# Kernel tuning notes

Hardware: AMD Instinct MI355X
Metric: run time of the kernel (lower is better)

Reference implementation:

```python
import jax, jax.numpy as jnp
import numpy as np

N = 100000   # nodes
E = 600000   # edges
IN = 128     # in_channels
H = 128      # hidden_channels
C = 47       # num_classes
L = 3        # num_layers
EPS = 1e-5   # batchnorm eps


def setup_inputs() -> dict:
    key = jax.random.key(0)
    ks = jax.random.split(key, 18)
    s = 0.05
    f = jnp.float32
    return {
        "x": jax.random.normal(ks[0], (N, IN), f),
        "in_W": jax.random.normal(ks[1], (IN, H), f) * s,
        "in_b": jnp.zeros((H,), f),
        "ibn_g": jnp.ones((H,), f),
        "ibn_b": jnp.zeros((H,), f),
        "ibn_m": jax.random.normal(ks[2], (H,), f) * 0.1,
        "ibn_v": jax.random.uniform(ks[3], (H,), f, 0.5, 1.5),
        "Wl": jax.random.normal(ks[4], (L, H, H), f) * s,   # SAGEConv lin_l (on aggregated neighbors)
        "bl": jnp.zeros((L, H), f),
        "Wr": jax.random.normal(ks[5], (L, H, H), f) * s,   # SAGEConv lin_r (root weight, no bias)
        "bn_g": jnp.ones((L, H), f),
        "bn_b": jnp.zeros((L, H), f),
        "bn_m": jax.random.normal(ks[6], (L, H), f) * 0.1,
        "bn_v": jax.random.uniform(ks[7], (L, H), f, 0.5, 1.5),
        "out_W": jax.random.normal(ks[8], (H, C), f) * s,
        "out_b": jnp.zeros((C,), f),
        "edge_index": jax.random.randint(ks[9], (2, E), 0, N),
    }


def _bn(h, g, b, m, v):
    # inference-mode BatchNorm1d with running stats
    return (h - m) * (g * jax.lax.rsqrt(v + EPS)) + b


def _sage(x, src, dst, Wl, bl, Wr):
    # mean aggregation of source features at destination nodes (PyG SAGEConv)
    msg = x[src]                                                   # [E, H] gather
    agg = jax.ops.segment_sum(msg, dst, num_segments=N)            # [N, H] scatter-add
    cnt = jax.ops.segment_sum(jnp.ones((src.shape[0],), x.dtype), dst, num_segments=N)
    agg = agg / jnp.maximum(cnt, 1.0)[:, None]                     # segment mean
    return agg @ Wl + bl + x @ Wr


def reference(x, in_W, in_b, ibn_g, ibn_b, ibn_m, ibn_v, Wl, bl, Wr,
              bn_g, bn_b, bn_m, bn_v, out_W, out_b, edge_index):
    src, dst = edge_index[0], edge_index[1]
    h = jax.nn.relu(_bn(x @ in_W + in_b, ibn_g, ibn_b, ibn_m, ibn_v))
    for l in range(L):  # small fixed layer count
        t = _sage(h, src, dst, Wl[l], bl[l], Wr[l])
        t = jax.nn.relu(_bn(t, bn_g[l], bn_b[l], bn_m[l], bn_v[l]))
        h = h + t  # residual
    return h @ out_W + out_b
```

## Files before the change

kernel.cpp:

```cpp
#include <hip/hip_runtime.h>
#include <math.h>

#define NN 100000
#define NE 600000
#define HD 128
#define NC 47
#define NL 3
#define BEPS 1e-5f

typedef unsigned short u16;
typedef unsigned int u32;
typedef __attribute__((ext_vector_type(8))) short bf16x8;
typedef __attribute__((ext_vector_type(4))) float f32x4;

__device__ inline u16 f2b(float f) {
  u32 u = __float_as_uint(f);
  u += 0x7fff + ((u >> 16) & 1);
  return (u16)(u >> 16);
}
__device__ inline float b2f(u16 us) { return __uint_as_float(((u32)us) << 16); }

__device__ inline void load_lds16(const void* g, void* l) {
  __builtin_amdgcn_global_load_lds(
      (const __attribute__((address_space(1))) void*)g,
      (__attribute__((address_space(3))) void*)l, 16, 0, 0);
}


__global__ void k_zero2(int* __restrict__ a, int* __restrict__ b) {
  int i = blockIdx.x * blockDim.x + threadIdx.x;
  if (i < NN) { a[i] = 0; b[i] = 0; }
}

__global__ void k_hist(const int* __restrict__ dst, int* __restrict__ cnt) {
  int e = blockIdx.x * blockDim.x + threadIdx.x;
  if (e < NE) atomicAdd(&cnt[dst[e]], 1);
}

__global__ void k_scan1(const int* __restrict__ cnt, int* __restrict__ rs, int* __restrict__ part) {
  __shared__ int s[256];
  int tid = threadIdx.x;
  int base = blockIdx.x * 1024;
  int i0 = base + tid * 4;
  int c[4];
#pragma unroll
  for (int j = 0; j < 4; j++) c[j] = (i0 + j < NN) ? cnt[i0 + j] : 0;
  int tsum = c[0] + c[1] + c[2] + c[3];
  s[tid] = tsum;
  __syncthreads();
  for (int off = 1; off < 256; off <<= 1) {
    int v = (tid >= off) ? s[tid - off] : 0;
    __syncthreads();
    s[tid] += v;
    __syncthreads();
  }
  int run = s[tid] - tsum;
#pragma unroll
  for (int j = 0; j < 4; j++) {
    run += c[j];
    if (i0 + j < NN) rs[i0 + j + 1] = run;
  }
  if (tid == 255) part[blockIdx.x] = s[255];
}

__global__ void k_scan2(const int* __restrict__ part, int* __restrict__ offs, int nb, int* __restrict__ rs) {
  __shared__ int s[128];
  int tid = threadIdx.x;
  int v = (tid < nb) ? part[tid] : 0;
  s[tid] = v;
  __syncthreads();
  for (int off = 1; off < 128; off <<= 1) {
    int u = (tid >= off) ? s[tid - off] : 0;
    __syncthreads();
    s[tid] += u;
    __syncthreads();
  }
  if (tid < nb) offs[tid] = s[tid] - v;
  if (tid == 0) rs[0] = 0;
}

__global__ void k_scan3(int* __restrict__ rs, const int* __restrict__ offs) {
  int off = offs[blockIdx.x];
  int base = blockIdx.x * 1024;
  int tid = threadIdx.x;
#pragma unroll
  for (int j = 0; j < 4; j++) {
    int i = base + tid * 4 + j;
    if (i < NN) rs[i + 1] += off;
  }
}

__global__ void k_scatter(const int* __restrict__ src, const int* __restrict__ dstA,
                          const int* __restrict__ rs, int* __restrict__ cur, int* __restrict__ ssrc) {
  int e = blockIdx.x * blockDim.x + threadIdx.x;
  if (e < NE) {
    int d = dstA[e];
    int p = atomicAdd(&cur[d], 1);
    ssrc[rs[d] + p] = src[e];
  }
}


__global__ void k_pack_all(const float* __restrict__ inW, const float* __restrict__ Wl,
                           const float* __restrict__ Wr, const float* __restrict__ oW,
                           u16* __restrict__ wpin, u16* __restrict__ wpl, u16* __restrict__ wpo) {
  int bid = blockIdx.x;
  int lane = threadIdx.x;
  int g = lane >> 4, r = lane & 15;
  union { u16 u[8]; uint4 v; } o;
  if (bid < 32) {
    int kt = bid >> 3, nt = bid & 7;
#pragma unroll
    for (int j = 0; j < 8; j++) {
      int k = kt * 32 + g * 8 + j, n = nt * 16 + r;
      o.u[j] = f2b(inW[k * HD + n]);
    }
    *(uint4*)(wpin + ((size_t)bid * 64 + lane) * 8) = o.v;
  } else if (bid < 224) {
    int b2 = bid - 32;
    int l = b2 >> 6, T = b2 & 63;
    int kt = T >> 3, nt = T & 7;
    const float* wl = Wl + (size_t)l * HD * HD;
    const float* wr = Wr + (size_t)l * HD * HD;
#pragma unroll
    for (int j = 0; j < 8; j++) {
      int k = kt * 32 + g * 8 + j, n = nt * 16 + r;
      o.u[j] = f2b(k < HD ? wl[k * HD + n] : wr[(k - HD) * HD + n]);
    }
    *(uint4*)(wpl + (((size_t)l * 64 + T) * 64 + lane) * 8) = o.v;
  } else {
    int T = bid - 224;
    int kt = T / 3, nt = T % 3;
#pragma unroll
    for (int j = 0; j < 8; j++) {
      int k = kt * 32 + g * 8 + j, n = nt * 16 + r;
      o.u[j] = (n < NC) ? f2b(oW[k * NC + n]) : (u16)0;
    }
    *(uint4*)(wpo + ((size_t)T * 64 + lane) * 8) = o.v;
  }
}


__global__ void k_agg(const u16* __restrict__ h, const int* __restrict__ rs,
                      const int* __restrict__ ssrc, u16* __restrict__ agg) {
  int gw = (blockIdx.x * blockDim.x + threadIdx.x) >> 6;
  int lane = threadIdx.x & 63;
  if (gw >= NN) return;
  int s = rs[gw], e = rs[gw + 1];
  const u32* h32 = (const u32*)h;
  float a0 = 0.f, a1 = 0.f, b0 = 0.f, b1 = 0.f;
  float c0 = 0.f, c1 = 0.f, d0 = 0.f, d1 = 0.f;
  int p = s;
  for (; p + 4 <= e; p += 4) {
    int n0 = ssrc[p], n1 = ssrc[p + 1], n2 = ssrc[p + 2], n3 = ssrc[p + 3];
    u32 u0 = h32[(size_t)n0 * 64 + lane];
    u32 u1 = h32[(size_t)n1 * 64 + lane];
    u32 u2 = h32[(size_t)n2 * 64 + lane];
    u32 u3 = h32[(size_t)n3 * 64 + lane];
    a0 += b2f((u16)(u0 & 0xffff)); a1 += b2f((u16)(u0 >> 16));
    b0 += b2f((u16)(u1 & 0xffff)); b1 += b2f((u16)(u1 >> 16));
    c0 += b2f((u16)(u2 & 0xffff)); c1 += b2f((u16)(u2 >> 16));
    d0 += b2f((u16)(u3 & 0xffff)); d1 += b2f((u16)(u3 >> 16));
  }
  if (p + 2 <= e) {
    int n0 = ssrc[p], n1 = ssrc[p + 1];
    u32 u0 = h32[(size_t)n0 * 64 + lane];
    u32 u1 = h32[(size_t)n1 * 64 + lane];
    a0 += b2f((u16)(u0 & 0xffff)); a1 += b2f((u16)(u0 >> 16));
    b0 += b2f((u16)(u1 & 0xffff)); b1 += b2f((u16)(u1 >> 16));
    p += 2;
  }
  if (p < e) {
    int n0 = ssrc[p];
    u32 u0 = h32[(size_t)n0 * 64 + lane];
    a0 += b2f((u16)(u0 & 0xffff)); a1 += b2f((u16)(u0 >> 16));
  }
  a0 += b0 + c0 + d0;
  a1 += b1 + c1 + d1;
  float inv = 1.0f / (float)max(e - s, 1);
  u32 o = (u32)f2b(a0 * inv) | ((u32)f2b(a1 * inv) << 16);
  ((u32*)agg)[(size_t)gw * 64 + lane] = o;
}


template <int KS, int MODE>
__global__ __launch_bounds__(256, 4) void k_mm(
    const float* __restrict__ Af, const u16* __restrict__ A0, const u16* __restrict__ A1,
    const u16* __restrict__ Wp, u16* __restrict__ hout,
    const float* __restrict__ bias, const float* __restrict__ g,
    const float* __restrict__ bb, const float* __restrict__ m,
    const float* __restrict__ v) {
  __shared__ __align__(1024) char As_raw[64 * KS * 64];
  __shared__ float sc_s[HD], sh_s[HD];
  int tid = threadIdx.x;
  int lane = tid & 63;
  int w = tid >> 6;
  long rbase = (long)blockIdx.x * 64;

  if (tid < HD) {
    float sc = g[tid] * rsqrtf(v[tid] + BEPS);
    sc_s[tid] = sc;
    sh_s[tid] = (bias[tid] - m[tid]) * sc + bb[tid];
  }

  if constexpr (MODE == 1) {
#pragma unroll
    for (int t = 0; t < 8; t++) {
      int op = w * 8 + t;
      int rowL = op * 2 + (lane >> 5);
      int p = lane & 31;
      int q = (p & 16) | ((p & 15) ^ (rowL & 15));
      long rg = rbase + rowL; if (rg > NN - 1) rg = NN - 1;
      const char* src = (q < 16)
          ? (const char*)A0 + rg * 256 + (size_t)q * 16
          : (const char*)A1 + rg * 256 + (size_t)(q - 16) * 16;
      load_lds16(src, As_raw + (size_t)op * 1024);
    }
  } else {
    int row = tid >> 2;
    int cq = (tid & 3) * 4;
    long rg = rbase + row; if (rg > NN - 1) rg = NN - 1;
    const float* srcp = Af + rg * HD + cq * 8;
#pragma unroll
    for (int ch = 0; ch < 4; ch++) {
      float4 f0 = *(const float4*)(srcp + ch * 8);
      float4 f1 = *(const float4*)(srcp + ch * 8 + 4);
      union { u16 u[8]; uint4 v4; } o;
      o.u[0] = f2b(f0.x); o.u[1] = f2b(f0.y); o.u[2] = f2b(f0.z); o.u[3] = f2b(f0.w);
      o.u[4] = f2b(f1.x); o.u[5] = f2b(f1.y); o.u[6] = f2b(f1.z); o.u[7] = f2b(f1.w);
      int q = cq + ch;
      int p = q ^ (row & 15);
      *(uint4*)(As_raw + (size_t)row * 256 + (size_t)p * 16) = o.v4;
    }
  }
  __syncthreads();

  int nb = w * 32;
  f32x4 acc[4][2];
#pragma unroll
  for (int mi = 0; mi < 4; mi++)
#pragma unroll
    for (int ni = 0; ni < 2; ni++) acc[mi][ni] = (f32x4)(0.0f);

#pragma unroll
  for (int kt = 0; kt < KS; kt++) {
    bf16x8 bfr[2];
#pragma unroll
    for (int ni = 0; ni < 2; ni++)
      bfr[ni] = *(const bf16x8*)(Wp + (((size_t)kt * 8 + (w * 2 + ni)) * 64 + lane) * 8);
#pragma unroll
    for (int mi = 0; mi < 4; mi++) {
      int row = mi * 16 + (lane & 15);
      int slot = kt * 4 + (lane >> 4);
      int p = (slot & ~15) | ((slot & 15) ^ (row & 15));
      bf16x8 afr = *(const bf16x8*)(As_raw + (size_t)row * (KS * 64) + (size_t)p * 16);
#pragma unroll
      for (int ni = 0; ni < 2; ni++)
        acc[mi][ni] = __builtin_amdgcn_mfma_f32_16x16x32_bf16(afr, bfr[ni], acc[mi][ni], 0, 0, 0);
    }
  }

#pragma unroll
  for (int mi = 0; mi < 4; mi++) {
#pragma unroll
    for (int ni = 0; ni < 2; ni++) {
      int c = nb + ni * 16 + (lane & 15);
      float sc = sc_s[c], sh = sh_s[c];
#pragma unroll
      for (int r = 0; r < 4; r++) {
        int rowL = mi * 16 + (lane >> 4) * 4 + r;
        long rg = rbase + rowL;
        if (rg >= NN) continue;
        float val = fmaxf(acc[mi][ni][r] * sc + sh, 0.f);
        if constexpr (MODE == 1) {
          int p = 16 | ((c >> 3) ^ (rowL & 15));
          u16 ho = *(const u16*)(As_raw + (size_t)rowL * 512 + (size_t)p * 16 + (c & 7) * 2);
          val += b2f(ho);
        }
        hout[rg * HD + c] = f2b(val);
      }
    }
  }
}


__global__ __launch_bounds__(256, 4) void k_outmm(const u16* __restrict__ h,
                                                  const u16* __restrict__ Wp,
                                                  const float* __restrict__ ob,
                                                  float* __restrict__ outp) {
  __shared__ __align__(1024) char As_raw[64 * 256];
  int tid = threadIdx.x;
  int lane = tid & 63;
  int w = tid >> 6;
  long rbase = (long)blockIdx.x * 64;
#pragma unroll
  for (int t = 0; t < 4; t++) {
    int op = w * 4 + t;
    int rowL = op * 4 + (lane >> 4);
    int p = lane & 15;
    int q = p ^ (rowL & 15);
    long rg = rbase + rowL; if (rg > NN - 1) rg = NN - 1;
    load_lds16((const char*)h + rg * 256 + (size_t)q * 16, As_raw + (size_t)op * 1024);
  }
  __syncthreads();

  f32x4 acc[3];
#pragma unroll
  for (int nt = 0; nt < 3; nt++) acc[nt] = (f32x4)(0.0f);
  int rowb = w * 16;
#pragma unroll
  for (int kt = 0; kt < 4; kt++) {
    int row = rowb + (lane & 15);
    int slot = kt * 4 + (lane >> 4);
    int p = slot ^ (row & 15);
    bf16x8 afr = *(const bf16x8*)(As_raw + (size_t)row * 256 + (size_t)p * 16);
#pragma unroll
    for (int nt = 0; nt < 3; nt++) {
      bf16x8 bfr = *(const bf16x8*)(Wp + (((size_t)kt * 3 + nt) * 64 + lane) * 8);
      acc[nt] = __builtin_amdgcn_mfma_f32_16x16x32_bf16(afr, bfr, acc[nt], 0, 0, 0);
    }
  }
#pragma unroll
  for (int nt = 0; nt < 3; nt++) {
#pragma unroll
    for (int r = 0; r < 4; r++) {
      long rg = rbase + rowb + (lane >> 4) * 4 + r;
      int c = nt * 16 + (lane & 15);
      if (rg < NN && c < NC) outp[rg * NC + c] = acc[nt][r] + ob[c];
    }
  }
}


extern "C" void kernel_launch(void* const* d_in, const int* in_sizes, int n_in,
                              void* d_out, int out_size, void* d_ws, size_t ws_size,
                              hipStream_t stream) {
  const float* x     = (const float*)d_in[0];
  const float* in_W  = (const float*)d_in[1];
  const float* in_b  = (const float*)d_in[2];
  const float* ibn_g = (const float*)d_in[3];
  const float* ibn_b = (const float*)d_in[4];
  const float* ibn_m = (const float*)d_in[5];
  const float* ibn_v = (const float*)d_in[6];
  const float* Wl    = (const float*)d_in[7];
  const float* bl    = (const float*)d_in[8];
  const float* Wr    = (const float*)d_in[9];
  const float* bn_g  = (const float*)d_in[10];
  const float* bn_b  = (const float*)d_in[11];
  const float* bn_m  = (const float*)d_in[12];
  const float* bn_v  = (const float*)d_in[13];
  const float* oW    = (const float*)d_in[14];
  const float* ob    = (const float*)d_in[15];
  const int* ei      = (const int*)d_in[16];
  const int* srcA = ei;
  const int* dstA = ei + NE;
  float* outp = (float*)d_out;

  char* W = (char*)d_ws;
  u16* h    = (u16*)W;
  u16* agg  = (u16*)(W + 25600000);
  u16* wpin = (u16*)(W + 76800000);
  u16* wpl  = (u16*)(W + 76800000 + 32768);
  u16* wpo  = (u16*)(W + 76800000 + 32768 + 196608);
  int* rs   = (int*)(W + 77041664);
  int* cnt  = rs + (NN + 1);
  int* cur  = cnt + NN;
  int* ssrc = cur + NN;
  int* part = ssrc + NE;
  int* offs = part + 128;

  k_zero2<<<(NN + 255) / 256, 256, 0, stream>>>(cnt, cur);
  k_hist<<<(NE + 255) / 256, 256, 0, stream>>>(dstA, cnt);
  int nb1 = (NN + 1023) / 1024;
  k_scan1<<<nb1, 256, 0, stream>>>(cnt, rs, part);
  k_scan2<<<1, 128, 0, stream>>>(part, offs, nb1, rs);
  k_scan3<<<nb1, 256, 0, stream>>>(rs, offs);
  k_scatter<<<(NE + 255) / 256, 256, 0, stream>>>(srcA, dstA, rs, cur, ssrc);

  k_pack_all<<<236, 64, 0, stream>>>(in_W, Wl, Wr, oW, wpin, wpl, wpo);

  int gblocks = (NN + 63) / 64;
  k_mm<4, 0><<<gblocks, 256, 0, stream>>>(x, nullptr, nullptr, wpin, h,
                                          in_b, ibn_g, ibn_b, ibn_m, ibn_v);
  for (int l = 0; l < NL; ++l) {
    k_agg<<<NN / 4, 256, 0, stream>>>(h, rs, ssrc, agg);
    k_mm<8, 1><<<gblocks, 256, 0, stream>>>(nullptr, agg, h, wpl + (size_t)l * 64 * 512, h,
                                            bl + (size_t)l * HD, bn_g + (size_t)l * HD,
                                            bn_b + (size_t)l * HD, bn_m + (size_t)l * HD,
                                            bn_v + (size_t)l * HD);
  }
  k_outmm<<<gblocks, 256, 0, stream>>>(h, wpo, ob, outp);
}
```

Before: 381.6 us.

## Partition CSR build atomics by destination range and aggregate four nodes per wave

The histogram and scatter kernels now use grid-stride loops in which each of eight block groups handles only destinations in its own range of 12500 nodes. The intent is to localize atomics and writes per group, at the cost of every group reading the whole destination array. The aggregation kernel now processes four destination nodes per wavefront and interleaves their neighbor gathers to expose more memory-level parallelism. This adds divergence when the four nodes have very different degrees and reduces the wave count.

New measurement: 427.0 us. +11.9%, slower.

```diff
diff --git a/kernel.cpp b/kernel.cpp
--- a/kernel.cpp
+++ b/kernel.cpp
@@ -32,9 +32,16 @@
   if (i < NN) { a[i] = 0; b[i] = 0; }
 }
 
+#define DPG 12500
+
 __global__ void k_hist(const int* __restrict__ dst, int* __restrict__ cnt) {
-  int e = blockIdx.x * blockDim.x + threadIdx.x;
-  if (e < NE) atomicAdd(&cnt[dst[e]], 1);
+  int g = blockIdx.x & 7;
+  int lo = g * DPG, hi = lo + DPG;
+  int stride = (gridDim.x >> 3) * blockDim.x;
+  for (int e = (blockIdx.x >> 3) * blockDim.x + threadIdx.x; e < NE; e += stride) {
+    int d = dst[e];
+    if (d >= lo && d < hi) atomicAdd(&cnt[d], 1);
+  }
 }
 
 __global__ void k_scan1(const int* __restrict__ cnt, int* __restrict__ rs, int* __restrict__ part) {
@@ -92,11 +99,15 @@
 
 __global__ void k_scatter(const int* __restrict__ src, const int* __restrict__ dstA,
                           const int* __restrict__ rs, int* __restrict__ cur, int* __restrict__ ssrc) {
-  int e = blockIdx.x * blockDim.x + threadIdx.x;
-  if (e < NE) {
+  int g = blockIdx.x & 7;
+  int lo = g * DPG, hi = lo + DPG;
+  int stride = (gridDim.x >> 3) * blockDim.x;
+  for (int e = (blockIdx.x >> 3) * blockDim.x + threadIdx.x; e < NE; e += stride) {
     int d = dstA[e];
-    int p = atomicAdd(&cur[d], 1);
-    ssrc[rs[d] + p] = src[e];
+    if (d >= lo && d < hi) {
+      int p = atomicAdd(&cur[d], 1);
+      ssrc[rs[d] + p] = src[e];
+    }
   }
 }
 
@@ -143,43 +154,34 @@
 
 __global__ void k_agg(const u16* __restrict__ h, const int* __restrict__ rs,
                       const int* __restrict__ ssrc, u16* __restrict__ agg) {
-  int gw = (blockIdx.x * blockDim.x + threadIdx.x) >> 6;
+  int wv = (blockIdx.x * blockDim.x + threadIdx.x) >> 6;
   int lane = threadIdx.x & 63;
-  if (gw >= NN) return;
-  int s = rs[gw], e = rs[gw + 1];
+  int base = wv * 4;
+  if (base >= NN) return;
   const u32* h32 = (const u32*)h;
-  float a0 = 0.f, a1 = 0.f, b0 = 0.f, b1 = 0.f;
-  float c0 = 0.f, c1 = 0.f, d0 = 0.f, d1 = 0.f;
-  int p = s;
-  for (; p + 4 <= e; p += 4) {
-    int n0 = ssrc[p], n1 = ssrc[p + 1], n2 = ssrc[p + 2], n3 = ssrc[p + 3];
-    u32 u0 = h32[(size_t)n0 * 64 + lane];
-    u32 u1 = h32[(size_t)n1 * 64 + lane];
-    u32 u2 = h32[(size_t)n2 * 64 + lane];
-    u32 u3 = h32[(size_t)n3 * 64 + lane];
-    a0 += b2f((u16)(u0 & 0xffff)); a1 += b2f((u16)(u0 >> 16));
-    b0 += b2f((u16)(u1 & 0xffff)); b1 += b2f((u16)(u1 >> 16));
-    c0 += b2f((u16)(u2 & 0xffff)); c1 += b2f((u16)(u2 >> 16));
-    d0 += b2f((u16)(u3 & 0xffff)); d1 += b2f((u16)(u3 >> 16));
-  }
-  if (p + 2 <= e) {
-    int n0 = ssrc[p], n1 = ssrc[p + 1];
-    u32 u0 = h32[(size_t)n0 * 64 + lane];
-    u32 u1 = h32[(size_t)n1 * 64 + lane];
-    a0 += b2f((u16)(u0 & 0xffff)); a1 += b2f((u16)(u0 >> 16));
-    b0 += b2f((u16)(u1 & 0xffff)); b1 += b2f((u16)(u1 >> 16));
-    p += 2;
-  }
-  if (p < e) {
-    int n0 = ssrc[p];
-    u32 u0 = h32[(size_t)n0 * 64 + lane];
-    a0 += b2f((u16)(u0 & 0xffff)); a1 += b2f((u16)(u0 >> 16));
-  }
-  a0 += b0 + c0 + d0;
-  a1 += b1 + c1 + d1;
-  float inv = 1.0f / (float)max(e - s, 1);
-  u32 o = (u32)f2b(a0 * inv) | ((u32)f2b(a1 * inv) << 16);
-  ((u32*)agg)[(size_t)gw * 64 + lane] = o;
+  int s0 = rs[base], s1 = rs[base + 1], s2 = rs[base + 2], s3 = rs[base + 3], s4 = rs[base + 4];
+  int l0 = s1 - s0, l1 = s2 - s1, l2 = s3 - s2, l3 = s4 - s3;
+  int maxl = max(max(l0, l1), max(l2, l3));
+  float a0 = 0.f, A0 = 0.f, a1 = 0.f, A1 = 0.f, a2 = 0.f, A2 = 0.f, a3 = 0.f, A3 = 0.f;
+  for (int i = 0; i < maxl; ++i) {
+    u32 u0, u1, u2, u3;
+    bool c0 = i < l0, c1 = i < l1, c2 = i < l2, c3 = i < l3;
+    if (c0) { int n = ssrc[s0 + i]; u0 = h32[(size_t)n * 64 + lane]; }
+    if (c1) { int n = ssrc[s1 + i]; u1 = h32[(size_t)n * 64 + lane]; }
+    if (c2) { int n = ssrc[s2 + i]; u2 = h32[(size_t)n * 64 + lane]; }
+    if (c3) { int n = ssrc[s3 + i]; u3 = h32[(size_t)n * 64 + lane]; }
+    if (c0) { a0 += b2f((u16)(u0 & 0xffff)); A0 += b2f((u16)(u0 >> 16)); }
+    if (c1) { a1 += b2f((u16)(u1 & 0xffff)); A1 += b2f((u16)(u1 >> 16)); }
+    if (c2) { a2 += b2f((u16)(u2 & 0xffff)); A2 += b2f((u16)(u2 >> 16)); }
+    if (c3) { a3 += b2f((u16)(u3 & 0xffff)); A3 += b2f((u16)(u3 >> 16)); }
+  }
+  u32* ag32 = (u32*)agg;
+  float i0 = 1.0f / (float)max(l0, 1), i1 = 1.0f / (float)max(l1, 1);
+  float i2 = 1.0f / (float)max(l2, 1), i3 = 1.0f / (float)max(l3, 1);
+  ag32[(size_t)(base + 0) * 64 + lane] = (u32)f2b(a0 * i0) | ((u32)f2b(A0 * i0) << 16);
+  ag32[(size_t)(base + 1) * 64 + lane] = (u32)f2b(a1 * i1) | ((u32)f2b(A1 * i1) << 16);
+  ag32[(size_t)(base + 2) * 64 + lane] = (u32)f2b(a2 * i2) | ((u32)f2b(A2 * i2) << 16);
+  ag32[(size_t)(base + 3) * 64 + lane] = (u32)f2b(a3 * i3) | ((u32)f2b(A3 * i3) << 16);
 }
 
 
@@ -370,12 +372,12 @@
   int* offs = part + 128;
 
   k_zero2<<<(NN + 255) / 256, 256, 0, stream>>>(cnt, cur);
-  k_hist<<<(NE + 255) / 256, 256, 0, stream>>>(dstA, cnt);
+  k_hist<<<2048, 256, 0, stream>>>(dstA, cnt);
   int nb1 = (NN + 1023) / 1024;
   k_scan1<<<nb1, 256, 0, stream>>>(cnt, rs, part);
   k_scan2<<<1, 128, 0, stream>>>(part, offs, nb1, rs);
   k_scan3<<<nb1, 256, 0, stream>>>(rs, offs);
-  k_scatter<<<(NE + 255) / 256, 256, 0, stream>>>(srcA, dstA, rs, cur, ssrc);
+  k_scatter<<<2048, 256, 0, stream>>>(srcA, dstA, rs, cur, ssrc);
 
   k_pack_all<<<236, 64, 0, stream>>>(in_W, Wl, Wr, oW, wpin, wpl, wpo);
 
@@ -383,7 +385,7 @@
   k_mm<4, 0><<<gblocks, 256, 0, stream>>>(x, nullptr, nullptr, wpin, h,
                                           in_b, ibn_g, ibn_b, ibn_m, ibn_v);
   for (int l = 0; l < NL; ++l) {
-    k_agg<<<NN / 4, 256, 0, stream>>>(h, rs, ssrc, agg);
+    k_agg<<<(NN / 4 + 1023) / 1024 * 256, 256, 0, stream>>>(h, rs, ssrc, agg);
     k_mm<8, 1><<<gblocks, 256, 0, stream>>>(nullptr, agg, h, wpl + (size_t)l * 64 * 512, h,
                                             bl + (size_t)l * HD, bn_g + (size_t)l * HD,
                                             bn_b + (size_t)l * HD, bn_m + (size_t)l * HD,
```
